# Kernel tuning notes

Hardware: AMD Instinct MI355X
Metric: run time of the kernel (lower is better)

## Reference

```python
import jax, jax.numpy as jnp
import numpy as np

N = 50000      # nodes
E = 800000     # edges (before self loops)
NF = 4         # node feature dim
EF = 4         # edge feature dim
EMB = 16       # joint embedding dim
HID = 64       # hidden dim
OUT = 128      # output dim
H = 4          # heads (layers 0,1); last layer has 1 head
NEG_SLOPE = 0.2


def setup_inputs() -> dict:
    key = jax.random.key(0)
    ks = jax.random.split(key, 20)
    in0 = NF + EMB  # 20

    def lin(k, o, i):
        return (jax.random.normal(k, (o, i), jnp.float32) * np.float32(1.0 / np.sqrt(i)))

    return {
        'x': jax.random.normal(ks[0], (N, NF), jnp.float32),
        'edge_index': jax.random.randint(ks[1], (2, E), 0, N, dtype=jnp.int32),
        'edge_attr': jax.random.normal(ks[2], (E, EF), jnp.float32),
        'joint_types': jax.random.randint(ks[3], (N,), 0, 17, dtype=jnp.int32),
        'emb_table': jax.random.normal(ks[4], (17, EMB), jnp.float32) * 0.1,
        'W0': lin(ks[5], H * HID, in0),
        'a_src0': jax.random.normal(ks[6], (H, HID), jnp.float32) * 0.1,
        'a_dst0': jax.random.normal(ks[7], (H, HID), jnp.float32) * 0.1,
        'We0': lin(ks[8], H, EF),
        'W1': lin(ks[9], H * HID, HID),
        'a_src1': jax.random.normal(ks[10], (H, HID), jnp.float32) * 0.1,
        'a_dst1': jax.random.normal(ks[11], (H, HID), jnp.float32) * 0.1,
        'We1': lin(ks[12], H, EF),
        'W2': lin(ks[13], 1 * OUT, HID),
        'a_src2': jax.random.normal(ks[14], (1, OUT), jnp.float32) * 0.1,
        'a_dst2': jax.random.normal(ks[15], (1, OUT), jnp.float32) * 0.1,
        'We2': lin(ks[16], 1, EF),
    }


def gat_layer(x, src, dst, eattr, W, a_src, a_dst, We, num_nodes):
    # x: [N, F_in]; W: [H*C, F_in]; a_src/a_dst: [H, C]; We: [H, EF]
    Hh, C = a_src.shape
    h = (x @ W.T).reshape(num_nodes, Hh, C)  # [N, H, C]
    # per-node attention scores, gathered per edge (same math as per-edge dot)
    s_i = jnp.einsum('nhc,hc->nh', h, a_src)  # applied to x_i = x[dst]
    s_j = jnp.einsum('nhc,hc->nh', h, a_dst)  # applied to x_j = x[src]
    alpha = s_i[dst] + s_j[src] + eattr @ We.T  # [Etot, H]
    alpha = jax.nn.leaky_relu(alpha, NEG_SLOPE)
    # faithful to torch.softmax(alpha, dim=0): GLOBAL softmax over all edges per head
    alpha = jax.nn.softmax(alpha, axis=0)
    msgs = h[src] * alpha[:, :, None]  # [Etot, H, C]
    out = jax.ops.segment_sum(msgs, dst, num_segments=num_nodes)  # aggr='add'
    return out.mean(axis=1)  # update(): mean over heads -> [N, C]


def reference(x, edge_index, edge_attr, joint_types, emb_table,
              W0, a_src0, a_dst0, We0,
              W1, a_src1, a_dst1, We1,
              W2, a_src2, a_dst2, We2):
    num_nodes = x.shape[0]
    # add self loops (edge_attr fill 0.0)
    loops = jnp.arange(num_nodes, dtype=edge_index.dtype)
    src = jnp.concatenate([edge_index[0], loops])
    dst = jnp.concatenate([edge_index[1], loops])
    eattr = jnp.concatenate([edge_attr, jnp.zeros((num_nodes, edge_attr.shape[1]), edge_attr.dtype)], axis=0)

    h = jnp.concatenate([x, emb_table[joint_types]], axis=-1)  # [N, 20]
    h = gat_layer(h, src, dst, eattr, W0, a_src0, a_dst0, We0, num_nodes)
    h = jax.nn.elu(h)  # dropout is identity in eval mode
    h = gat_layer(h, src, dst, eattr, W1, a_src1, a_dst1, We1, num_nodes)
    h = jax.nn.elu(h)
    h = gat_layer(h, src, dst, eattr, W2, a_src2, a_dst2, We2, num_nodes)
    return h  # [N, OUT]
```

## Files before the change

kernel.cpp:

```cpp
#include <hip/hip_runtime.h>
#include <math.h>

#define NN 50000
#define EE 800000
#define EEN (EE+NN)
#define STRIDE 64
#define NFEAT 4
#define EFEAT 4
#define EMBD 16
#define IN0 20
#define HIDD 64
#define OUTD 128

__device__ __forceinline__ unsigned short f2bf(float f){
  unsigned u = __float_as_uint(f);
  return (unsigned short)((u + 0x7FFFu + ((u>>16)&1u)) >> 16);
}
__device__ __forceinline__ float bfl(unsigned u){ return __uint_as_float(u<<16); }
__device__ __forceinline__ float bfh(unsigned u){ return __uint_as_float(u & 0xFFFF0000u); }

template<int V> struct ldt;
template<> struct ldt<4>{ using T = uint2; };
template<> struct ldt<2>{ using T = unsigned int; };

__global__ void k_init(int* fill){
  int i = blockIdx.x*blockDim.x + threadIdx.x;
  if (i < NN) fill[i]=0;
}

__global__ void k_scatter(const int* __restrict__ ei, int* fill,
                          int2* __restrict__ col){
  int idx = blockIdx.x*blockDim.x + threadIdx.x;
  if (idx < EE){
    int d = ei[EE+idx];
    int pos = atomicAdd(&fill[d],1);
    col[d*STRIDE + 1 + pos] = make_int2(ei[idx], idx);
  } else if (idx < EEN){
    int n = idx-EE;
    col[n*STRIDE] = make_int2(n, EE+n);
  }
}

template<int F_IN,int HH,int CC>
__device__ __forceinline__ void av_one(const float* W, const float* asrc,
                                       const float* adst, float* av, int tid){
  if (tid >= HH*F_IN) return;
  int h = tid / F_IN, f = tid % F_IN;
  float s1=0.f, s2=0.f;
  for (int c=0;c<CC;c++){
    float wv = W[(size_t)(h*CC+c)*F_IN+f];
    s1 += asrc[h*CC+c]*wv;
    s2 += adst[h*CC+c]*wv;
  }
  av[tid] = s1;
  av[HH*F_IN+tid] = s2;
}
__global__ void k_av3(const float* W0, const float* as0, const float* ad0, float* av0,
                      const float* W1, const float* as1, const float* ad1, float* av1,
                      const float* W2, const float* as2, const float* ad2, float* av2,
                      float* zred){
  int tid = threadIdx.x;
  if      (blockIdx.x==0){ av_one<IN0,4,64> (W0, as0, ad0, av0, tid); if (tid<24) zred[tid]=0.f; }
  else if (blockIdx.x==1) av_one<64,4,64>  (W1, as1, ad1, av1, tid);
  else                    av_one<64,1,128> (W2, as2, ad2, av2, tid);
}

template<int K,int NCOL,int HH,bool CONCAT>
__global__ __launch_bounds__(256)
void k_gemm(const float* __restrict__ xin, const int* __restrict__ jt,
            const float* __restrict__ emb, const float* __restrict__ W,
            const float* __restrict__ avp, unsigned short* __restrict__ hout,
            float* __restrict__ si, float* __restrict__ sj){
  constexpr int PITCH = 132;
  __shared__ float xT[K*PITCH];
  __shared__ float wT[K*PITCH];
  __shared__ float EMBL[CONCAT ? 17*EMBD : 1];
  int tid = threadIdx.x;
  int rbase = blockIdx.x*128, cbase = blockIdx.y*128;
  if (CONCAT){
    for (int i=tid; i<17*EMBD; i+=256) EMBL[i]=emb[i];
    __syncthreads();
    if (tid < 128){
      int row = tid;
      int gr = rbase+row; if (gr >= NN) gr = NN-1;
      float4 v = ((const float4*)xin)[gr];
      xT[0*PITCH+row]=v.x; xT[1*PITCH+row]=v.y;
      xT[2*PITCH+row]=v.z; xT[3*PITCH+row]=v.w;
      int j = jt[gr];
      #pragma unroll
      for (int k=0;k<EMBD;k++) xT[(NFEAT+k)*PITCH+row] = EMBL[j*EMBD+k];
    } else {
      int col = tid-128;
      const float4* wp = (const float4*)(W + (size_t)(cbase+col)*K);
      #pragma unroll
      for (int k4=0;k4<K/4;k4++){
        float4 v = wp[k4];
        wT[(4*k4+0)*PITCH+col]=v.x; wT[(4*k4+1)*PITCH+col]=v.y;
        wT[(4*k4+2)*PITCH+col]=v.z; wT[(4*k4+3)*PITCH+col]=v.w;
      }
    }
  } else {
    constexpr int K4 = K/4;
    for (int i=tid; i<128*K4; i+=256){
      int row = i/K4, k4 = i%K4;
      int gr = rbase+row; if (gr >= NN) gr = NN-1;
      float4 v = ((const float4*)xin)[(size_t)gr*K4 + k4];
      xT[(4*k4+0)*PITCH+row]=v.x; xT[(4*k4+1)*PITCH+row]=v.y;
      xT[(4*k4+2)*PITCH+row]=v.z; xT[(4*k4+3)*PITCH+row]=v.w;
    }
    for (int i=tid; i<128*K4; i+=256){
      int col = i/K4, k4 = i%K4;
      float4 v = ((const float4*)W)[(size_t)(cbase+col)*K4 + k4];
      wT[(4*k4+0)*PITCH+col]=v.x; wT[(4*k4+1)*PITCH+col]=v.y;
      wT[(4*k4+2)*PITCH+col]=v.z; wT[(4*k4+3)*PITCH+col]=v.w;
    }
  }
  __syncthreads();
  int lane = tid & 63, w = tid >> 6;
  int r0 = (w>>1)*64 + (lane&7)*8;
  int c0 = (w&1)*64 + (lane>>3)*8;
  float acc[8][8];
  #pragma unroll
  for (int i=0;i<8;i++)
    #pragma unroll
    for (int j=0;j<8;j++) acc[i][j]=0.f;
  #pragma unroll 4
  for (int k=0;k<K;k++){
    float a[8], b[8];
    *(float4*)&a[0] = *(const float4*)&xT[k*PITCH + r0];
    *(float4*)&a[4] = *(const float4*)&xT[k*PITCH + r0 + 4];
    *(float4*)&b[0] = *(const float4*)&wT[k*PITCH + c0];
    *(float4*)&b[4] = *(const float4*)&wT[k*PITCH + c0 + 4];
    #pragma unroll
    for (int i=0;i<8;i++)
      #pragma unroll
      for (int j=0;j<8;j++) acc[i][j] += a[i]*b[j];
  }
  if (blockIdx.y==0 && tid < 128){
    int row = tid, gr = rbase+row;
    if (gr < NN){
      #pragma unroll
      for (int h=0;h<HH;h++){
        float a=0.f, b=0.f;
        for (int k=0;k<K;k++){
          float xv = xT[k*PITCH+row];
          a += xv*avp[h*K+k];
          b += xv*avp[HH*K+h*K+k];
        }
        si[(size_t)gr*HH+h]=a;
        sj[(size_t)gr*HH+h]=b;
      }
    }
  }
  #pragma unroll
  for (int i=0;i<8;i++){
    int n = rbase + r0 + i;
    if (n < NN){
      uint4 o;
      o.x = (unsigned)f2bf(acc[i][0]) | ((unsigned)f2bf(acc[i][1])<<16);
      o.y = (unsigned)f2bf(acc[i][2]) | ((unsigned)f2bf(acc[i][3])<<16);
      o.z = (unsigned)f2bf(acc[i][4]) | ((unsigned)f2bf(acc[i][5])<<16);
      o.w = (unsigned)f2bf(acc[i][6]) | ((unsigned)f2bf(acc[i][7])<<16);
      *(uint4*)(hout + (size_t)n*NCOL + cbase + c0) = o;
    }
  }
}

template<int HH>
__global__ void k_edge(const int* __restrict__ ei, const float* __restrict__ eattr,
                       const float* __restrict__ We, const float* __restrict__ si,
                       const float* __restrict__ sj,
                       float* __restrict__ pp, float* __restrict__ zred){
  int idx = blockIdx.x*blockDim.x + threadIdx.x;
  float z[HH];
  #pragma unroll
  for (int h=0;h<HH;h++) z[h]=0.f;
  if (idx < EE){
    int s = ei[idx], d = ei[EE+idx];
    const float4 ea = ((const float4*)eattr)[idx];
    if (HH==4){
      float4 siv = ((const float4*)si)[d];
      float4 sjv = ((const float4*)sj)[s];
      float te[4] = {siv.x+sjv.x, siv.y+sjv.y, siv.z+sjv.z, siv.w+sjv.w};
      float pv[4];
      #pragma unroll
      for (int h=0;h<4;h++){
        float t = te[h] + ea.x*We[h*EFEAT+0] + ea.y*We[h*EFEAT+1]
                        + ea.z*We[h*EFEAT+2] + ea.w*We[h*EFEAT+3];
        t = (t>0.f)? t : 0.2f*t;
        float p = expf(t);
        z[h]=p; pv[h]=p;
      }
      ((float4*)pp)[idx] = make_float4(pv[0],pv[1],pv[2],pv[3]);
    } else {
      float t = si[d] + sj[s]
              + ea.x*We[0] + ea.y*We[1] + ea.z*We[2] + ea.w*We[3];
      t = (t>0.f)? t : 0.2f*t;
      float p = expf(t);
      z[0]=p;
      pp[idx] = p;
    }
  } else if (idx < EEN){
    int n = idx-EE;
    if (HH==4){
      float4 siv = ((const float4*)si)[n];
      float4 sjv = ((const float4*)sj)[n];
      float te[4] = {siv.x+sjv.x, siv.y+sjv.y, siv.z+sjv.z, siv.w+sjv.w};
      float pv[4];
      #pragma unroll
      for (int h=0;h<4;h++){
        float t = te[h];
        t = (t>0.f)? t : 0.2f*t;
        float p = expf(t);
        z[h]=p; pv[h]=p;
      }
      ((float4*)pp)[idx] = make_float4(pv[0],pv[1],pv[2],pv[3]);
    } else {
      float t = si[n]+sj[n];
      t = (t>0.f)? t : 0.2f*t;
      float p = expf(t);
      z[0]=p;
      pp[idx]=p;
    }
  }
  __shared__ float zs[4][HH];
  #pragma unroll
  for (int h=0;h<HH;h++){
    float v=z[h];
    #pragma unroll
    for (int off=32; off>0; off>>=1) v += __shfl_xor(v,off,64);
    if ((threadIdx.x&63)==0) zs[threadIdx.x>>6][h]=v;
  }
  __syncthreads();
  if (threadIdx.x < HH){
    float tot = zs[0][threadIdx.x]+zs[1][threadIdx.x]
              + zs[2][threadIdx.x]+zs[3][threadIdx.x];
    atomicAdd(&zred[threadIdx.x], tot);
  }
}

template<int HH,int CC,bool DO_ELU>
__global__ __launch_bounds__(256)
void k_agg(const unsigned short* __restrict__ hb, const float* __restrict__ pp,
           const float* __restrict__ zred, const int* __restrict__ fill,
           const int2* __restrict__ col, float* __restrict__ outp){
  constexpr int HC = HH*CC;
  constexpr int V  = HC/64;
  using LT = typename ldt<V>::T;
  int wave = threadIdx.x>>6, lane = threadIdx.x&63;
  int n = blockIdx.x*4 + wave;
  int hd = (lane*V)/CC;
  float invZ = 1.0f/zred[hd];
  float acc[V];
  #pragma unroll
  for (int v=0;v<V;v++) acc[v]=0.f;
  auto mac = [&](float p, LT h){
    if constexpr (V==4){
      acc[0] += p*bfl(h.x); acc[1] += p*bfh(h.x);
      acc[2] += p*bfl(h.y); acc[3] += p*bfh(h.y);
    } else {
      acc[0] += p*bfl(h);   acc[1] += p*bfh(h);
    }
  };
  int beg = n*STRIDE, end = beg + 1 + fill[n];
  int i = beg;
  for (; i+8<=end; i+=8){
    int2 ce[8]; float p[8]; LT h[8];
    #pragma unroll
    for (int k=0;k<8;k++) ce[k]=col[i+k];
    #pragma unroll
    for (int k=0;k<8;k++) p[k]=pp[(size_t)ce[k].y*HH+hd];
    #pragma unroll
    for (int k=0;k<8;k++) h[k]=((const LT*)(hb + (size_t)ce[k].x*HC))[lane];
    #pragma unroll
    for (int k=0;k<8;k++) mac(p[k], h[k]);
  }
  for (; i<end; i++){
    int2 ce = col[i];
    float p = pp[(size_t)ce.y*HH+hd];
    LT h = ((const LT*)(hb + (size_t)ce.x*HC))[lane];
    mac(p, h);
  }
  #pragma unroll
  for (int v=0;v<V;v++) acc[v] *= invZ;
  if (HH==4){
    #pragma unroll
    for (int off=16; off<64; off<<=1){
      #pragma unroll
      for (int v=0;v<V;v++) acc[v] += __shfl_xor(acc[v], off, 64);
    }
    if (lane < 16){
      float4 o;
      o.x=0.25f*acc[0]; o.y=0.25f*acc[1]; o.z=0.25f*acc[2]; o.w=0.25f*acc[3];
      if (DO_ELU){
        o.x = (o.x>0.f)? o.x : expm1f(o.x);
        o.y = (o.y>0.f)? o.y : expm1f(o.y);
        o.z = (o.z>0.f)? o.z : expm1f(o.z);
        o.w = (o.w>0.f)? o.w : expm1f(o.w);
      }
      ((float4*)outp)[(size_t)n*(CC/4)+lane] = o;
    }
  } else {
    float2 o; o.x=acc[0]; o.y=acc[1];
    if (DO_ELU){
      o.x = (o.x>0.f)? o.x : expm1f(o.x);
      o.y = (o.y>0.f)? o.y : expm1f(o.y);
    }
    ((float2*)outp)[(size_t)n*(CC/2)+lane] = o;
  }
}

extern "C" void kernel_launch(void* const* d_in, const int* in_sizes, int n_in,
                              void* d_out, int out_size, void* d_ws, size_t ws_size,
                              hipStream_t stream){
  const float* x    = (const float*)d_in[0];
  const int*   ei   = (const int*)d_in[1];
  const float* eatt = (const float*)d_in[2];
  const int*   jt   = (const int*)d_in[3];
  const float* emb  = (const float*)d_in[4];
  const float* W0   = (const float*)d_in[5];
  const float* as0  = (const float*)d_in[6];
  const float* ad0  = (const float*)d_in[7];
  const float* We0  = (const float*)d_in[8];
  const float* W1   = (const float*)d_in[9];
  const float* as1  = (const float*)d_in[10];
  const float* ad1  = (const float*)d_in[11];
  const float* We1  = (const float*)d_in[12];
  const float* W2   = (const float*)d_in[13];
  const float* as2  = (const float*)d_in[14];
  const float* ad2  = (const float*)d_in[15];
  const float* We2  = (const float*)d_in[16];
  float* out = (float*)d_out;

  char* p = (char*)d_ws;
  auto alloc = [&](size_t bytes)->char*{
    char* r = p; p += (bytes + 255) & ~(size_t)255; return r;
  };
  unsigned short* hbuf = (unsigned short*)alloc((size_t)NN*256*2);
  float* x1     = (float*)alloc((size_t)NN*64*4);
  float* x2     = (float*)alloc((size_t)NN*64*4);
  float* si     = (float*)alloc((size_t)NN*4*4);
  float* sj     = (float*)alloc((size_t)NN*4*4);
  float* pp     = (float*)alloc((size_t)EEN*4*4);
  int*   fill   = (int*)alloc((size_t)NN*4);
  int2*  col    = (int2*)alloc((size_t)NN*STRIDE*8);
  float* av0    = (float*)alloc(512*4);
  float* av1    = (float*)alloc(512*4);
  float* av2    = (float*)alloc(512*4);
  float* zred   = (float*)alloc(3*8*4);

  k_init   <<<dim3((NN+255)/256),  256, 0, stream>>>(fill);
  k_scatter<<<dim3((EEN+255)/256), 256, 0, stream>>>(ei, fill, col);
  k_av3    <<<dim3(3),             256, 0, stream>>>(W0,as0,ad0,av0, W1,as1,ad1,av1,
                                                     W2,as2,ad2,av2, zred);

  dim3 gg01((NN+127)/128, 2);
  dim3 gg2 ((NN+127)/128, 1);
  dim3 egrid((EEN+255)/256);
  dim3 agrid(NN/4);

  k_gemm<IN0,256,4,true> <<<gg01, 256, 0, stream>>>(x, jt, emb, W0, av0, hbuf, si, sj);
  k_edge<4>              <<<egrid,256, 0, stream>>>(ei, eatt, We0, si, sj, pp, zred+0);
  k_agg<4,64,true>       <<<agrid,256, 0, stream>>>(hbuf, pp, zred+0, fill, col, x1);

  k_gemm<64,256,4,false> <<<gg01, 256, 0, stream>>>(x1, jt, emb, W1, av1, hbuf, si, sj);
  k_edge<4>              <<<egrid,256, 0, stream>>>(ei, eatt, We1, si, sj, pp, zred+8);
  k_agg<4,64,true>       <<<agrid,256, 0, stream>>>(hbuf, pp, zred+8, fill, col, x2);

  k_gemm<64,128,1,false> <<<gg2,  256, 0, stream>>>(x2, jt, emb, W2, av2, hbuf, si, sj);
  k_edge<1>              <<<egrid,256, 0, stream>>>(ei, eatt, We2, si, sj, pp, zred+16);
  k_agg<1,128,false>     <<<agrid,256, 0, stream>>>(hbuf, pp, zred+16, fill, col, out);
}
```

Measured before the change: 582.3 us.

## Store edge attention weights in CSR slot order to make aggregation reads contiguous

The scatter kernel now records each edge's slot position in the padded per-destination adjacency. The edge kernel writes its exponentiated scores directly into that slot, so the aggregation kernel reads scores sequentially instead of gathering them by edge id. The adjacency array shrinks from int2 to int. In exchange, the edge kernel does scattered writes and an extra epos read, and the score buffer grows to the padded NN*STRIDE size.

```diff
diff --git a/kernel.cpp b/kernel.cpp
--- a/kernel.cpp
+++ b/kernel.cpp
@@ -29,15 +29,16 @@
 }
 
 __global__ void k_scatter(const int* __restrict__ ei, int* fill,
-                          int2* __restrict__ col){
+                          int* __restrict__ col, int* __restrict__ epos){
   int idx = blockIdx.x*blockDim.x + threadIdx.x;
   if (idx < EE){
     int d = ei[EE+idx];
     int pos = atomicAdd(&fill[d],1);
-    col[d*STRIDE + 1 + pos] = make_int2(ei[idx], idx);
+    col[d*STRIDE + 1 + pos] = ei[idx];
+    epos[idx] = d*STRIDE + 1 + pos;
   } else if (idx < EEN){
     int n = idx-EE;
-    col[n*STRIDE] = make_int2(n, EE+n);
+    col[n*STRIDE] = n;
   }
 }
 
@@ -169,7 +170,7 @@
 template<int HH>
 __global__ void k_edge(const int* __restrict__ ei, const float* __restrict__ eattr,
                        const float* __restrict__ We, const float* __restrict__ si,
-                       const float* __restrict__ sj,
+                       const float* __restrict__ sj, const int* __restrict__ epos,
                        float* __restrict__ pp, float* __restrict__ zred){
   int idx = blockIdx.x*blockDim.x + threadIdx.x;
   float z[HH];
@@ -178,6 +179,7 @@
   if (idx < EE){
     int s = ei[idx], d = ei[EE+idx];
     const float4 ea = ((const float4*)eattr)[idx];
+    int pos = epos[idx];
     if (HH==4){
       float4 siv = ((const float4*)si)[d];
       float4 sjv = ((const float4*)sj)[s];
@@ -191,17 +193,18 @@
         float p = expf(t);
         z[h]=p; pv[h]=p;
       }
-      ((float4*)pp)[idx] = make_float4(pv[0],pv[1],pv[2],pv[3]);
+      ((float4*)pp)[pos] = make_float4(pv[0],pv[1],pv[2],pv[3]);
     } else {
       float t = si[d] + sj[s]
               + ea.x*We[0] + ea.y*We[1] + ea.z*We[2] + ea.w*We[3];
       t = (t>0.f)? t : 0.2f*t;
       float p = expf(t);
       z[0]=p;
-      pp[idx] = p;
+      pp[pos] = p;
     }
   } else if (idx < EEN){
     int n = idx-EE;
+    int pos = n*STRIDE;
     if (HH==4){
       float4 siv = ((const float4*)si)[n];
       float4 sjv = ((const float4*)sj)[n];
@@ -214,13 +217,13 @@
         float p = expf(t);
         z[h]=p; pv[h]=p;
       }
-      ((float4*)pp)[idx] = make_float4(pv[0],pv[1],pv[2],pv[3]);
+      ((float4*)pp)[pos] = make_float4(pv[0],pv[1],pv[2],pv[3]);
     } else {
       float t = si[n]+sj[n];
       t = (t>0.f)? t : 0.2f*t;
       float p = expf(t);
       z[0]=p;
-      pp[idx]=p;
+      pp[pos]=p;
     }
   }
   __shared__ float zs[4][HH];
@@ -243,7 +246,7 @@
 __global__ __launch_bounds__(256)
 void k_agg(const unsigned short* __restrict__ hb, const float* __restrict__ pp,
            const float* __restrict__ zred, const int* __restrict__ fill,
-           const int2* __restrict__ col, float* __restrict__ outp){
+           const int* __restrict__ col, float* __restrict__ outp){
   constexpr int HC = HH*CC;
   constexpr int V  = HC/64;
   using LT = typename ldt<V>::T;
@@ -265,20 +268,21 @@
   int beg = n*STRIDE, end = beg + 1 + fill[n];
   int i = beg;
   for (; i+8<=end; i+=8){
-    int2 ce[8]; float p[8]; LT h[8];
-    #pragma unroll
-    for (int k=0;k<8;k++) ce[k]=col[i+k];
-    #pragma unroll
-    for (int k=0;k<8;k++) p[k]=pp[(size_t)ce[k].y*HH+hd];
-    #pragma unroll
-    for (int k=0;k<8;k++) h[k]=((const LT*)(hb + (size_t)ce[k].x*HC))[lane];
+    int sr[8]; float p[8]; LT h[8];
+    #pragma unroll
+    for (int k=0;k<8;k++) sr[k]=col[i+k];
+    #pragma unroll
+    for (int k=0;k<8;k++)
+      p[k] = (HH==4) ? pp[(size_t)(i+k)*4+hd] : pp[i+k];
+    #pragma unroll
+    for (int k=0;k<8;k++) h[k]=((const LT*)(hb + (size_t)sr[k]*HC))[lane];
     #pragma unroll
     for (int k=0;k<8;k++) mac(p[k], h[k]);
   }
   for (; i<end; i++){
-    int2 ce = col[i];
-    float p = pp[(size_t)ce.y*HH+hd];
-    LT h = ((const LT*)(hb + (size_t)ce.x*HC))[lane];
+    int sr = col[i];
+    float p = (HH==4) ? pp[(size_t)i*4+hd] : pp[i];
+    LT h = ((const LT*)(hb + (size_t)sr*HC))[lane];
     mac(p, h);
   }
   #pragma unroll
@@ -341,16 +345,17 @@
   float* x2     = (float*)alloc((size_t)NN*64*4);
   float* si     = (float*)alloc((size_t)NN*4*4);
   float* sj     = (float*)alloc((size_t)NN*4*4);
-  float* pp     = (float*)alloc((size_t)EEN*4*4);
+  float* pp     = (float*)alloc((size_t)NN*STRIDE*16);
   int*   fill   = (int*)alloc((size_t)NN*4);
-  int2*  col    = (int2*)alloc((size_t)NN*STRIDE*8);
+  int*   col    = (int*)alloc((size_t)NN*STRIDE*4);
+  int*   epos   = (int*)alloc((size_t)EE*4);
   float* av0    = (float*)alloc(512*4);
   float* av1    = (float*)alloc(512*4);
   float* av2    = (float*)alloc(512*4);
   float* zred   = (float*)alloc(3*8*4);
 
   k_init   <<<dim3((NN+255)/256),  256, 0, stream>>>(fill);
-  k_scatter<<<dim3((EEN+255)/256), 256, 0, stream>>>(ei, fill, col);
+  k_scatter<<<dim3((EEN+255)/256), 256, 0, stream>>>(ei, fill, col, epos);
   k_av3    <<<dim3(3),             256, 0, stream>>>(W0,as0,ad0,av0, W1,as1,ad1,av1,
                                                      W2,as2,ad2,av2, zred);
 
@@ -360,14 +365,14 @@
   dim3 agrid(NN/4);
 
   k_gemm<IN0,256,4,true> <<<gg01, 256, 0, stream>>>(x, jt, emb, W0, av0, hbuf, si, sj);
-  k_edge<4>              <<<egrid,256, 0, stream>>>(ei, eatt, We0, si, sj, pp, zred+0);
+  k_edge<4>              <<<egrid,256, 0, stream>>>(ei, eatt, We0, si, sj, epos, pp, zred+0);
   k_agg<4,64,true>       <<<agrid,256, 0, stream>>>(hbuf, pp, zred+0, fill, col, x1);
 
   k_gemm<64,256,4,false> <<<gg01, 256, 0, stream>>>(x1, jt, emb, W1, av1, hbuf, si, sj);
-  k_edge<4>              <<<egrid,256, 0, stream>>>(ei, eatt, We1, si, sj, pp, zred+8);
+  k_edge<4>              <<<egrid,256, 0, stream>>>(ei, eatt, We1, si, sj, epos, pp, zred+8);
   k_agg<4,64,true>       <<<agrid,256, 0, stream>>>(hbuf, pp, zred+8, fill, col, x2);
 
   k_gemm<64,128,1,false> <<<gg2,  256, 0, stream>>>(x2, jt, emb, W2, av2, hbuf, si, sj);
-  k_edge<1>              <<<egrid,256, 0, stream>>>(ei, eatt, We2, si, sj, pp, zred+16);
+  k_edge<1>              <<<egrid,256, 0, stream>>>(ei, eatt, We2, si, sj, epos, pp, zred+16);
   k_agg<1,128,false>     <<<agrid,256, 0, stream>>>(hbuf, pp, zred+16, fill, col, out);
 }
```

Measured after the change: 540.1 us. -7.2%, faster.
